# Optimization experiments

Hardware: AMD Instinct MI355X
Metric: run time of the kernel (lower is better)

## Reference

```python
import jax, jax.numpy as jnp
import numpy as np
from jax import lax

TAU = 2.0      # tau_s
V_TH = 0.5     # spike threshold
ALPHA = 2.0    # ATan surrogate width

@jax.custom_vjp
def spike_fn(v):
    return (v >= V_TH).astype(v.dtype)

def _spike_fwd(v):
    return spike_fn(v), v

def _spike_bwd(v, g):
    sg = (ALPHA / 2.0) / (1.0 + (jnp.pi / 2.0 * ALPHA * (v - V_TH)) ** 2)
    return (g * sg,)

spike_fn.defvjp(_spike_fwd, _spike_bwd)

T, B, S = 4, 128, 64
D_STATE = D_TAU = D_EVENT = 3136
FUSION, HIDDEN, LAST = 512, 512, 18

def setup_inputs() -> dict:
    key = jax.random.key(0)
    ks = jax.random.split(key, 10)
    def w(k, i, o):
        return jax.random.normal(k, (i, o), jnp.float32) / np.sqrt(i)
    return {
        'state_embedding': jax.random.normal(ks[0], (T, B, D_STATE), jnp.float32),
        'tau_embedding': jax.random.normal(ks[1], (T, B * S, D_TAU), jnp.float32),
        'eventspikes_embedding': jax.random.normal(ks[2], (T, B, D_EVENT), jnp.float32),
        'W_prox': w(ks[3], D_STATE, FUSION),
        'W_dist': w(ks[4], D_TAU, FUSION),
        'W_trunk': w(ks[5], D_EVENT, FUSION),
        'W1': w(ks[6], FUSION, HIDDEN),
        'b1': jnp.zeros((HIDDEN,), jnp.float32),
        'W2': w(ks[7], HIDDEN, LAST),
        'b2': jnp.zeros((LAST,), jnp.float32),
    }

def reference(state_embedding, tau_embedding, eventspikes_embedding,
              W_prox, W_dist, W_trunk, W1, b1, W2, b2):
    t_win, bsz, _ = state_embedding.shape
    ssz = tau_embedding.shape[1] // bsz
    fsz = W_prox.shape[1]
    hsz = W1.shape[1]

    def step(carry, xs):
        p, d, t, soma, lif_mem = carry
        se, te, ee = xs
        prox = (se @ W_prox)[:, None, :]              # [B,1,F]
        dist = (te @ W_dist).reshape(bsz, ssz, fsz)   # [B,S,F]
        trunk = (ee @ W_trunk)[:, None, :]            # [B,1,F]
        # multi-compartment LIF integration
        p = p + (prox - p) / TAU
        d = d + (dist - d) / TAU
        t = t + (trunk - t) / TAU
        soma = soma + (p * d + t - soma) / TAU        # [B,S,F]
        s = spike_fn(soma)
        soma = soma * (1.0 - s)
        emb = s.reshape(bsz * ssz, fsz)
        # _last: Linear -> LIF -> Linear
        h = emb @ W1 + b1
        lif_mem = lif_mem + (h - lif_mem) / TAU
        hs = spike_fn(lif_mem)
        lif_mem = lif_mem * (1.0 - hs)
        out = hs @ W2 + b2                            # [B*S, LAST]
        return (p, d, t, soma, lif_mem), out

    z = jnp.zeros
    init = (z((bsz, 1, fsz)), z((bsz, ssz, fsz)), z((bsz, 1, fsz)),
            z((bsz, ssz, fsz)), z((bsz * ssz, hsz)))
    _, outs = lax.scan(step, init, (state_embedding, tau_embedding, eventspikes_embedding))
    q = outs.mean(0)                                  # average over time window
    return q.reshape(bsz, ssz, -1).transpose(0, 2, 1)  # [B, LAST, S]
```

## Files before the change

### kernel.cpp

```cpp
#include <hip/hip_runtime.h>
#include <stdint.h>

typedef __attribute__((ext_vector_type(4))) float f32x4;

#define T_WIN 4
#define BSZ   128
#define SSZ   64
#define DDIM  3136
#define FDIM  512
#define HDIM  512
#define LDIM  18
#define ROWS  8192
#define KB    32

struct GArgs { const void* A; const float* B; float* C; int M; };

template<int AMODE>
__global__ __launch_bounds__(256, 2) void sgemm_kernel(GArgs g0, GArgs g1, GArgs g2,
                                                       int N, int K,
                                                       uint64_t bm_lo, uint64_t bm_hi) {
  GArgs g = g0;
  if (blockIdx.z == 1) g = g1;
  else if (blockIdx.z == 2) g = g2;
  const int m0 = blockIdx.x * 128;
  if (m0 >= g.M) return;
  const int n0 = blockIdx.y * 128;

  __shared__ float sA[KB][132];
  __shared__ float sB[KB][132];

  const int tid = threadIdx.x;
  const int tx = tid & 15;
  const int ty = tid >> 4;

  const int am  = tid >> 1;
  const int aks = (tid & 1) * 16;
  const int br  = tid >> 3;
  const int bcs = (tid & 7) * 16;

  const float*   Af = (const float*)g.A;
  const uint8_t* A8 = (const uint8_t*)g.A;

  float run[8][8], cur[8][8];
#pragma unroll
  for (int i = 0; i < 8; i++)
#pragma unroll
    for (int j = 0; j < 8; j++) { run[i][j] = 0.f; cur[i][j] = 0.f; }

  const int KT = K / KB;
  for (int kt = 0; kt < KT; kt++) {
    const int k0 = kt * KB;
    f32x4 av[4];
    if (AMODE == 0) {
      const float* ap = Af + (size_t)(m0 + am) * K + k0 + aks;
#pragma unroll
      for (int c = 0; c < 4; c++) av[c] = *(const f32x4*)(ap + 4 * c);
    } else {
      const uint8_t* ap = A8 + (size_t)(m0 + am) * K + k0 + aks;
      uint4 wrd = *(const uint4*)ap;
      uint32_t u[4] = {wrd.x, wrd.y, wrd.z, wrd.w};
#pragma unroll
      for (int c = 0; c < 4; c++) {
        av[c][0] = (float)(u[c] & 255u);
        av[c][1] = (float)((u[c] >> 8) & 255u);
        av[c][2] = (float)((u[c] >> 16) & 255u);
        av[c][3] = (float)((u[c] >> 24) & 255u);
      }
    }
    f32x4 bv[4];
    const float* bp = g.B + (size_t)(k0 + br) * N + n0 + bcs;
#pragma unroll
    for (int c = 0; c < 4; c++) bv[c] = *(const f32x4*)(bp + 4 * c);

    __syncthreads();
#pragma unroll
    for (int c = 0; c < 4; c++)
#pragma unroll
      for (int j = 0; j < 4; j++)
        sA[aks + 4 * c + j][am] = av[c][j];
#pragma unroll
    for (int c = 0; c < 4; c++)
      *(f32x4*)&sB[br][bcs + 4 * c] = bv[c];
    __syncthreads();

    const bool fl = (kt < 64) ? (((bm_lo >> kt) & 1ull) != 0)
                              : (((bm_hi >> (kt - 64)) & 1ull) != 0);
    if (fl) {
#pragma unroll
      for (int i = 0; i < 8; i++)
#pragma unroll
        for (int j = 0; j < 8; j++) {
          run[i][j] = __fadd_rn(run[i][j], cur[i][j]);
          cur[i][j] = 0.f;
        }
    }

#pragma unroll 4
    for (int k = 0; k < KB; k++) {
      f32x4 a0 = *(const f32x4*)&sA[k][ty * 8];
      f32x4 a1 = *(const f32x4*)&sA[k][ty * 8 + 4];
      f32x4 b0 = *(const f32x4*)&sB[k][tx * 8];
      f32x4 b1 = *(const f32x4*)&sB[k][tx * 8 + 4];
      float a[8] = {a0[0], a0[1], a0[2], a0[3], a1[0], a1[1], a1[2], a1[3]};
      float b[8] = {b0[0], b0[1], b0[2], b0[3], b1[0], b1[1], b1[2], b1[3]};
#pragma unroll
      for (int i = 0; i < 8; i++)
#pragma unroll
        for (int j = 0; j < 8; j++)
          cur[i][j] = __fmaf_rn(a[i], b[j], cur[i][j]);
    }
  }

#pragma unroll
  for (int i = 0; i < 8; i++) {
    size_t rowoff = (size_t)(m0 + ty * 8 + i) * N + n0 + tx * 8;
#pragma unroll
    for (int j = 0; j < 2; j++) {
      f32x4 v;
#pragma unroll
      for (int c = 0; c < 4; c++)
        v[c] = __fadd_rn(run[i][4 * j + c], cur[i][4 * j + c]);
      *(f32x4*)(g.C + rowoff + 4 * j) = v;
    }
  }
}

__global__ __launch_bounds__(256) void filter_pt_kernel(const float* __restrict__ prox,
                                                        const float* __restrict__ trunk,
                                                        float* __restrict__ P,
                                                        float* __restrict__ Tf) {
  int idx = blockIdx.x * 256 + threadIdx.x;
  int b = idx >> 7;
  int fc = (idx & 127) << 2;
  f32x4 p = {0.f, 0.f, 0.f, 0.f}, t = {0.f, 0.f, 0.f, 0.f};
  for (int tt = 0; tt < T_WIN; tt++) {
    size_t o = (size_t)(tt * BSZ + b) * FDIM + fc;
    f32x4 x = *(const f32x4*)&prox[o];
    f32x4 y = *(const f32x4*)&trunk[o];
#pragma unroll
    for (int c = 0; c < 4; c++) {
      p[c] = __fadd_rn(p[c], __fmul_rn(__fsub_rn(x[c], p[c]), 0.5f));
      t[c] = __fadd_rn(t[c], __fmul_rn(__fsub_rn(y[c], t[c]), 0.5f));
    }
    *(f32x4*)&P[o] = p;
    *(f32x4*)&Tf[o] = t;
  }
}

__global__ __launch_bounds__(256) void lif_soma_kernel(const float* __restrict__ dist,
                                                       const float* __restrict__ P,
                                                       const float* __restrict__ Tf,
                                                       uint8_t* __restrict__ emb) {
  int idx = blockIdx.x * 256 + threadIdx.x;
  int r = idx >> 7;
  int fc = (idx & 127) << 2;
  int b = r >> 6;
  f32x4 d = {0.f, 0.f, 0.f, 0.f}, soma = {0.f, 0.f, 0.f, 0.f};
#pragma unroll
  for (int t = 0; t < T_WIN; t++) {
    f32x4 x  = *(const f32x4*)&dist[(size_t)(t * ROWS + r) * FDIM + fc];
    f32x4 pv = *(const f32x4*)&P[(size_t)(t * BSZ + b) * FDIM + fc];
    f32x4 tv = *(const f32x4*)&Tf[(size_t)(t * BSZ + b) * FDIM + fc];
    uint32_t bits = 0;
#pragma unroll
    for (int c = 0; c < 4; c++) {
      d[c] = __fadd_rn(d[c], __fmul_rn(__fsub_rn(x[c], d[c]), 0.5f));
      float pd = __fmul_rn(pv[c], d[c]);
      float u  = __fadd_rn(pd, tv[c]);
      float w  = __fsub_rn(u, soma[c]);
      soma[c] = __fadd_rn(soma[c], __fmul_rn(w, 0.5f));
      if (soma[c] >= 0.5f) { bits |= (1u << (8 * c)); soma[c] = 0.f; }
    }
    *(uint32_t*)&emb[(size_t)(t * ROWS + r) * FDIM + fc] = bits;
  }
}

__global__ __launch_bounds__(256) void lif_hidden_kernel(const float* __restrict__ H,
                                                         const float* __restrict__ b1,
                                                         uint8_t* __restrict__ cnt) {
  int idx = blockIdx.x * 256 + threadIdx.x;
  int r = idx >> 7;
  int fc = (idx & 127) << 2;
  f32x4 bb = *(const f32x4*)&b1[fc];
  f32x4 lif = {0.f, 0.f, 0.f, 0.f};
  uint32_t counts = 0;
#pragma unroll
  for (int t = 0; t < T_WIN; t++) {
    f32x4 h = *(const f32x4*)&H[(size_t)(t * ROWS + r) * FDIM + fc];
#pragma unroll
    for (int c = 0; c < 4; c++) {
      float hv = __fadd_rn(h[c], bb[c]);
      lif[c] = __fadd_rn(lif[c], __fmul_rn(__fsub_rn(hv, lif[c]), 0.5f));
      if (lif[c] >= 0.5f) { counts += (1u << (8 * c)); lif[c] = 0.f; }
    }
  }
  *(uint32_t*)&cnt[(size_t)r * FDIM + fc] = counts;
}

__global__ __launch_bounds__(256) void out_kernel(const uint8_t* __restrict__ cnt,
                                                  const float* __restrict__ W2,
                                                  const float* __restrict__ b2,
                                                  float* __restrict__ out) {
  int idx = blockIdx.x * 256 + threadIdx.x;
  int r = idx / LDIM;
  int j = idx - r * LDIM;
  const uint8_t* crow = cnt + (size_t)r * HDIM;
  float acc = 0.f;
  for (int k = 0; k < HDIM; k++) {
    uint32_t c = crow[k];
    if (c) acc = __fmaf_rn((float)c * 0.25f, W2[k * LDIM + j], acc);
  }
  int b = r >> 6, s = r & 63;
  out[(size_t)b * (LDIM * SSZ) + j * SSZ + s] = __fadd_rn(acc, b2[j]);
}


extern "C" void kernel_launch(void* const* d_in, const int* in_sizes, int n_in,
                              void* d_out, int out_size, void* d_ws, size_t ws_size,
                              hipStream_t stream) {
  const float* se     = (const float*)d_in[0];
  const float* te     = (const float*)d_in[1];
  const float* ee     = (const float*)d_in[2];
  const float* Wprox  = (const float*)d_in[3];
  const float* Wdist  = (const float*)d_in[4];
  const float* Wtrunk = (const float*)d_in[5];
  const float* W1     = (const float*)d_in[6];
  const float* b1     = (const float*)d_in[7];
  const float* W2     = (const float*)d_in[8];
  const float* b2     = (const float*)d_in[9];

  char* ws = (char*)d_ws;
  float*   dist_all  = (float*)(ws);
  uint8_t* emb8      = (uint8_t*)(ws + 67108864);
  uint8_t* cnt8      = (uint8_t*)(ws + 83886080);
  float*   prox_raw  = (float*)(ws + 88080384);
  float*   trunk_raw = (float*)(ws + 89128960);
  float*   P         = (float*)(ws + 90177536);
  float*   Tf        = (float*)(ws + 91226112);

  const uint64_t bm3136_lo = (1ull << 12) | (1ull << 24) | (1ull << 36) |
                             (1ull << 48) | (1ull << 60);
  const uint64_t bm3136_hi = (1ull << (72 - 64)) | (1ull << (84 - 64)) | (1ull << (91 - 64));
  const uint64_t bm512_lo = (1ull << 8);

  GArgs gd{te, Wdist, dist_all, T_WIN * ROWS};
  GArgs gp{se, Wprox, prox_raw, T_WIN * BSZ};
  GArgs gt{ee, Wtrunk, trunk_raw, T_WIN * BSZ};
  sgemm_kernel<0><<<dim3(256, 4, 3), 256, 0, stream>>>(gd, gp, gt, FDIM, DDIM,
                                                       bm3136_lo, bm3136_hi);

  filter_pt_kernel<<<64, 256, 0, stream>>>(prox_raw, trunk_raw, P, Tf);

  lif_soma_kernel<<<4096, 256, 0, stream>>>(dist_all, P, Tf, emb8);

  GArgs gh{emb8, W1, dist_all, T_WIN * ROWS};
  sgemm_kernel<1><<<dim3(256, 4, 1), 256, 0, stream>>>(gh, gh, gh, HDIM, FDIM,
                                                       bm512_lo, 0ull);

  lif_hidden_kernel<<<4096, 256, 0, stream>>>(dist_all, b1, cnt8);

  out_kernel<<<576, 256, 0, stream>>>(cnt8, W2, b2, (float*)d_out);
}
```

Baseline: 2.291 ms.

## Split SGEMMs into K-chunk passes with 128-thread 16x8 microtiles

Replaces the single-launch SGEMM, which kept separate running and current accumulators flushed on a bitmask of K tiles, with a series of K-range passes. Each pass writes or read-modify-writes the output in global memory, which mimics chunked summation order. Blocks shrink to 128 threads with 16x8 register microtiles and K-tile 16. The out kernel now reads 16 count bytes per vector load. This removes the double accumulator register pressure and raises per-thread reuse, but adds repeated global read/write of the large output per pass and many more launches.

Measured after the change: 2.403 ms. 4.9% more time.

```diff
diff --git a/kernel.cpp b/kernel.cpp
--- a/kernel.cpp
+++ b/kernel.cpp
@@ -11,14 +11,13 @@
 #define HDIM  512
 #define LDIM  18
 #define ROWS  8192
-#define KB    32
+#define KB    16
 
 struct GArgs { const void* A; const float* B; float* C; int M; };
 
-template<int AMODE>
-__global__ __launch_bounds__(256, 2) void sgemm_kernel(GArgs g0, GArgs g1, GArgs g2,
-                                                       int N, int K,
-                                                       uint64_t bm_lo, uint64_t bm_hi) {
+template<int AMODE, int FIRST>
+__global__ __launch_bounds__(128, 2) void sgemm_pass(GArgs g0, GArgs g1, GArgs g2,
+                                                     int N, int K, int ks, int ke) {
   GArgs g = g0;
   if (blockIdx.z == 1) g = g1;
   else if (blockIdx.z == 2) g = g2;
@@ -26,38 +25,34 @@
   if (m0 >= g.M) return;
   const int n0 = blockIdx.y * 128;
 
-  __shared__ float sA[KB][132];
+  __shared__ float sA[KB][256];
   __shared__ float sB[KB][132];
 
   const int tid = threadIdx.x;
   const int tx = tid & 15;
   const int ty = tid >> 4;
 
-  const int am  = tid >> 1;
-  const int aks = (tid & 1) * 16;
-  const int br  = tid >> 3;
-  const int bcs = (tid & 7) * 16;
+  const int am = tid;
+  const int br = tid >> 3;
+  const int bc = (tid & 7) * 16;
 
   const float*   Af = (const float*)g.A;
   const uint8_t* A8 = (const uint8_t*)g.A;
 
-  float run[8][8], cur[8][8];
-#pragma unroll
-  for (int i = 0; i < 8; i++)
-#pragma unroll
-    for (int j = 0; j < 8; j++) { run[i][j] = 0.f; cur[i][j] = 0.f; }
-
-  const int KT = K / KB;
-  for (int kt = 0; kt < KT; kt++) {
-    const int k0 = kt * KB;
+  float acc[16][8];
+#pragma unroll
+  for (int i = 0; i < 16; i++)
+#pragma unroll
+    for (int j = 0; j < 8; j++) acc[i][j] = 0.f;
+
+  for (int k0 = ks; k0 < ke; k0 += KB) {
     f32x4 av[4];
     if (AMODE == 0) {
-      const float* ap = Af + (size_t)(m0 + am) * K + k0 + aks;
+      const float* ap = Af + (size_t)(m0 + am) * K + k0;
 #pragma unroll
       for (int c = 0; c < 4; c++) av[c] = *(const f32x4*)(ap + 4 * c);
     } else {
-      const uint8_t* ap = A8 + (size_t)(m0 + am) * K + k0 + aks;
-      uint4 wrd = *(const uint4*)ap;
+      uint4 wrd = *(const uint4*)(A8 + (size_t)(m0 + am) * K + k0);
       uint32_t u[4] = {wrd.x, wrd.y, wrd.z, wrd.w};
 #pragma unroll
       for (int c = 0; c < 4; c++) {
@@ -68,7 +63,7 @@
       }
     }
     f32x4 bv[4];
-    const float* bp = g.B + (size_t)(k0 + br) * N + n0 + bcs;
+    const float* bp = g.B + (size_t)(k0 + br) * N + n0 + bc;
 #pragma unroll
     for (int c = 0; c < 4; c++) bv[c] = *(const f32x4*)(bp + 4 * c);
 
@@ -77,50 +72,46 @@
     for (int c = 0; c < 4; c++)
 #pragma unroll
       for (int j = 0; j < 4; j++)
-        sA[aks + 4 * c + j][am] = av[c][j];
+        sA[4 * c + j][am] = av[c][j];
 #pragma unroll
     for (int c = 0; c < 4; c++)
-      *(f32x4*)&sB[br][bcs + 4 * c] = bv[c];
+      *(f32x4*)&sB[br][bc + 4 * c] = bv[c];
     __syncthreads();
 
-    const bool fl = (kt < 64) ? (((bm_lo >> kt) & 1ull) != 0)
-                              : (((bm_hi >> (kt - 64)) & 1ull) != 0);
-    if (fl) {
-#pragma unroll
-      for (int i = 0; i < 8; i++)
-#pragma unroll
-        for (int j = 0; j < 8; j++) {
-          run[i][j] = __fadd_rn(run[i][j], cur[i][j]);
-          cur[i][j] = 0.f;
-        }
-    }
-
-#pragma unroll 4
+#pragma unroll 2
     for (int k = 0; k < KB; k++) {
-      f32x4 a0 = *(const f32x4*)&sA[k][ty * 8];
-      f32x4 a1 = *(const f32x4*)&sA[k][ty * 8 + 4];
-      f32x4 b0 = *(const f32x4*)&sB[k][tx * 8];
-      f32x4 b1 = *(const f32x4*)&sB[k][tx * 8 + 4];
-      float a[8] = {a0[0], a0[1], a0[2], a0[3], a1[0], a1[1], a1[2], a1[3]};
-      float b[8] = {b0[0], b0[1], b0[2], b0[3], b1[0], b1[1], b1[2], b1[3]};
-#pragma unroll
-      for (int i = 0; i < 8; i++)
+      f32x4 a0 = *(const f32x4*)&sA[k][ty * 16];
+      f32x4 a1 = *(const f32x4*)&sA[k][ty * 16 + 4];
+      f32x4 a2 = *(const f32x4*)&sA[k][ty * 16 + 8];
+      f32x4 a3 = *(const f32x4*)&sA[k][ty * 16 + 12];
+      f32x4 b0 = *(const f32x4*)&sB[k][tx * 4];
+      f32x4 b1 = *(const f32x4*)&sB[k][64 + tx * 4];
+      float a[16] = {a0[0], a0[1], a0[2], a0[3], a1[0], a1[1], a1[2], a1[3],
+                     a2[0], a2[1], a2[2], a2[3], a3[0], a3[1], a3[2], a3[3]};
+      float b[8]  = {b0[0], b0[1], b0[2], b0[3], b1[0], b1[1], b1[2], b1[3]};
+#pragma unroll
+      for (int i = 0; i < 16; i++)
 #pragma unroll
         for (int j = 0; j < 8; j++)
-          cur[i][j] = __fmaf_rn(a[i], b[j], cur[i][j]);
-    }
-  }
-
-#pragma unroll
-  for (int i = 0; i < 8; i++) {
-    size_t rowoff = (size_t)(m0 + ty * 8 + i) * N + n0 + tx * 8;
-#pragma unroll
-    for (int j = 0; j < 2; j++) {
-      f32x4 v;
-#pragma unroll
-      for (int c = 0; c < 4; c++)
-        v[c] = __fadd_rn(run[i][4 * j + c], cur[i][4 * j + c]);
-      *(f32x4*)(g.C + rowoff + 4 * j) = v;
+          acc[i][j] = __fmaf_rn(a[i], b[j], acc[i][j]);
+    }
+  }
+
+#pragma unroll
+  for (int i = 0; i < 16; i++) {
+    float* cp = g.C + (size_t)(m0 + ty * 16 + i) * N + n0;
+    f32x4 v0 = {acc[i][0], acc[i][1], acc[i][2], acc[i][3]};
+    f32x4 v1 = {acc[i][4], acc[i][5], acc[i][6], acc[i][7]};
+    if (FIRST) {
+      *(f32x4*)(cp + tx * 4) = v0;
+      *(f32x4*)(cp + 64 + tx * 4) = v1;
+    } else {
+      f32x4 o0 = *(const f32x4*)(cp + tx * 4);
+      f32x4 o1 = *(const f32x4*)(cp + 64 + tx * 4);
+#pragma unroll
+      for (int c = 0; c < 4; c++) { v0[c] = __fadd_rn(o0[c], v0[c]); v1[c] = __fadd_rn(o1[c], v1[c]); }
+      *(f32x4*)(cp + tx * 4) = v0;
+      *(f32x4*)(cp + 64 + tx * 4) = v1;
     }
   }
 }
@@ -204,11 +195,18 @@
   int idx = blockIdx.x * 256 + threadIdx.x;
   int r = idx / LDIM;
   int j = idx - r * LDIM;
-  const uint8_t* crow = cnt + (size_t)r * HDIM;
+  const uint4* crow = (const uint4*)(cnt + (size_t)r * HDIM);
   float acc = 0.f;
-  for (int k = 0; k < HDIM; k++) {
-    uint32_t c = crow[k];
-    if (c) acc = __fmaf_rn((float)c * 0.25f, W2[k * LDIM + j], acc);
+  for (int q = 0; q < HDIM / 16; q++) {
+    uint4 wrd = crow[q];
+    uint32_t u[4] = {wrd.x, wrd.y, wrd.z, wrd.w};
+#pragma unroll
+    for (int wq = 0; wq < 4; wq++)
+#pragma unroll
+      for (int s = 0; s < 4; s++) {
+        uint32_t c = (u[wq] >> (8 * s)) & 255u;
+        if (c) acc = __fmaf_rn((float)c * 0.25f, W2[(16 * q + 4 * wq + s) * LDIM + j], acc);
+      }
   }
   int b = r >> 6, s = r & 63;
   out[(size_t)b * (LDIM * SSZ) + j * SSZ + s] = __fadd_rn(acc, b2[j]);
@@ -238,24 +236,28 @@
   float*   P         = (float*)(ws + 90177536);
   float*   Tf        = (float*)(ws + 91226112);
 
-  const uint64_t bm3136_lo = (1ull << 12) | (1ull << 24) | (1ull << 36) |
-                             (1ull << 48) | (1ull << 60);
-  const uint64_t bm3136_hi = (1ull << (72 - 64)) | (1ull << (84 - 64)) | (1ull << (91 - 64));
-  const uint64_t bm512_lo = (1ull << 8);
+  static const int KC[10] = {0, 384, 768, 1152, 1536, 1920, 2304, 2688, 2912, 3136};
 
   GArgs gd{te, Wdist, dist_all, T_WIN * ROWS};
   GArgs gp{se, Wprox, prox_raw, T_WIN * BSZ};
   GArgs gt{ee, Wtrunk, trunk_raw, T_WIN * BSZ};
-  sgemm_kernel<0><<<dim3(256, 4, 3), 256, 0, stream>>>(gd, gp, gt, FDIM, DDIM,
-                                                       bm3136_lo, bm3136_hi);
+  {
+    dim3 gg(256, 4, 3), bb(128);
+    sgemm_pass<0, 1><<<gg, bb, 0, stream>>>(gd, gp, gt, FDIM, DDIM, KC[0], KC[1]);
+    for (int p = 1; p < 9; p++)
+      sgemm_pass<0, 0><<<gg, bb, 0, stream>>>(gd, gp, gt, FDIM, DDIM, KC[p], KC[p + 1]);
+  }
 
   filter_pt_kernel<<<64, 256, 0, stream>>>(prox_raw, trunk_raw, P, Tf);
 
   lif_soma_kernel<<<4096, 256, 0, stream>>>(dist_all, P, Tf, emb8);
 
   GArgs gh{emb8, W1, dist_all, T_WIN * ROWS};
-  sgemm_kernel<1><<<dim3(256, 4, 1), 256, 0, stream>>>(gh, gh, gh, HDIM, FDIM,
-                                                       bm512_lo, 0ull);
+  {
+    dim3 gg(256, 4, 1), bb(128);
+    sgemm_pass<1, 1><<<gg, bb, 0, stream>>>(gh, gh, gh, HDIM, FDIM, 0, 256);
+    sgemm_pass<1, 0><<<gg, bb, 0, stream>>>(gh, gh, gh, HDIM, FDIM, 256, 512);
+  }
 
   lif_hidden_kernel<<<4096, 256, 0, stream>>>(dist_all, b1, cnt8);
 
```
